# Performance work log

Hardware: AMD Instinct MI355X
Metric: run time of the kernel (lower is better)

The kernel has to match this reference:

```python
import jax, jax.numpy as jnp
import numpy as np

NUM_HEADS = 16
NUM_KV_HEADS = 4
HEAD_DIM = 128
MIN_VALUE = -1e9  # fp32 branch of the torch code


def _rotate_half_interleaved(x):
    # stack([-x[...,1::2], x[...,::2]], -1).reshape_as(x)
    x_even = x[..., ::2]
    x_odd = x[..., 1::2]
    return jnp.stack([-x_odd, x_even], axis=-1).reshape(x.shape)


def setup_inputs() -> dict:
    key = jax.random.key(0)
    ks = jax.random.split(key, 7)
    B, S, D = 2, 2048, 2048
    hidden_states = jax.random.normal(ks[0], (B, S, D), dtype=jnp.float32)
    # realistic rope tables
    inv_freq = 1.0 / (100000.0 ** (np.arange(0, HEAD_DIM, 2, dtype=np.float32) / HEAD_DIM))
    t = np.arange(S, dtype=np.float32)
    freqs = np.outer(t, inv_freq)  # (S, HEAD_DIM/2)
    emb = np.repeat(freqs, 2, axis=-1)  # interleaved layout (S, HEAD_DIM)
    cos = jnp.asarray(np.cos(emb), dtype=jnp.float32)
    sin = jnp.asarray(np.sin(emb), dtype=jnp.float32)
    scale = 0.02
    Wq = jax.random.normal(ks[1], (D, D), dtype=jnp.float32) * scale
    Wk = jax.random.normal(ks[2], (D, NUM_KV_HEADS * HEAD_DIM), dtype=jnp.float32) * scale
    Wv = jax.random.normal(ks[3], (D, NUM_KV_HEADS * HEAD_DIM), dtype=jnp.float32) * scale
    Wo = jax.random.normal(ks[4], (D, D), dtype=jnp.float32) * scale
    return {"hidden_states": hidden_states, "cos": cos, "sin": sin,
            "Wq": Wq, "Wk": Wk, "Wv": Wv, "Wo": Wo}


def reference(hidden_states, cos, sin, Wq, Wk, Wv, Wo):
    B, S, D = hidden_states.shape
    H, KV, hd = NUM_HEADS, NUM_KV_HEADS, HEAD_DIM
    q = (hidden_states @ Wq).reshape(B, S, H, hd)
    k = (hidden_states @ Wk).reshape(B, S, KV, hd)
    v = (hidden_states @ Wv).reshape(B, S, KV, hd)

    # RoPE: cos/sin (S, hd) unsqueezed to (S, 1, hd) broadcasting over heads
    c = cos[:, None, :]
    s = sin[:, None, :]
    q = q * c + _rotate_half_interleaved(q) * s
    k = k * c + _rotate_half_interleaved(k) * s

    # repeat_kv (GQA expansion): (B,S,KV,hd) -> (B,S,H,hd)
    rep = H // KV
    k = jnp.repeat(k, rep, axis=2)
    v = jnp.repeat(v, rep, axis=2)

    scores = jnp.einsum('bqhd,bkhd->bhqk', q, k) / jnp.sqrt(jnp.float32(hd))
    causal = jnp.triu(jnp.ones((S, S), dtype=bool), k=1)
    scores = jnp.where(causal[None, None], scores + MIN_VALUE, scores)
    probs = jax.nn.softmax(scores, axis=-1)
    attn = jnp.einsum('bhqk,bkhd->bqhd', probs, v).reshape(B, S, D)
    out = attn @ Wo
    return out
```

## Files before the change

### kernel.cpp

```cpp
#include <hip/hip_runtime.h>

typedef unsigned short u16;
typedef unsigned int u32;
typedef __bf16 bf16x8 __attribute__((ext_vector_type(8)));
typedef float f32x4 __attribute__((ext_vector_type(4)));

__device__ __forceinline__ u16 f2bf(float f) {
  union { float f; u32 u; } v; v.f = f;
  u32 r = v.u + 0x7fffu + ((v.u >> 16) & 1u);
  return (u16)(r >> 16);
}

__device__ __forceinline__ bf16x8 ldb128(const u16* p) {
  return *reinterpret_cast<const bf16x8*>(p);
}

__device__ __forceinline__ f32x4 mfma16(bf16x8 a, bf16x8 b, f32x4 c) {
  return __builtin_amdgcn_mfma_f32_16x16x32_bf16(a, b, c, 0, 0, 0);
}

typedef const __attribute__((address_space(1))) u32* gas_p;
typedef __attribute__((address_space(3))) u32* las_p;
__device__ __forceinline__ void gld_lds16(const void* g, void* l) {
  __builtin_amdgcn_global_load_lds((gas_p)(unsigned long long)g,
                                   (las_p)(u32)(unsigned long long)l, 16, 0, 0);
}

__global__ __launch_bounds__(256) void cvt_f32_bf16(const float4* __restrict__ in,
                                                    uint2* __restrict__ out) {
  int i = blockIdx.x * 256 + threadIdx.x;
  float4 v = in[i];
  uint2 r;
  r.x = (u32)f2bf(v.x) | ((u32)f2bf(v.y) << 16);
  r.y = (u32)f2bf(v.z) | ((u32)f2bf(v.w) << 16);
  out[i] = r;
}

__global__ __launch_bounds__(256) void transp_cvt(const float* __restrict__ in,
                                                  u16* __restrict__ out, int R, int C) {
  __shared__ float tile[32][33];
  int n0 = blockIdx.x * 32, k0 = blockIdx.y * 32;
  int tx = threadIdx.x, ty = threadIdx.y;
#pragma unroll
  for (int i = 0; i < 32; i += 8) tile[ty + i][tx] = in[(k0 + ty + i) * C + n0 + tx];
  __syncthreads();
#pragma unroll
  for (int i = 0; i < 32; i += 8) out[(n0 + ty + i) * R + k0 + tx] = f2bf(tile[tx][ty + i]);
}

template<int BN, int WM, int WN, int MODE, int LOADS>
__global__ __launch_bounds__(512) void gemm_pipe(
    const u16* __restrict__ A, const u16* __restrict__ Bt,
    int M, int N, int K,
    const float* __restrict__ cosb, const float* __restrict__ sinb,
    u16* __restrict__ Qb, u16* __restrict__ Kb, u16* __restrict__ Vt,
    float* __restrict__ outf) {
  constexpr int BM = 256;
  constexpr int WTM = BM / WM;
  constexpr int WTN = BN / WN;
  constexpr int MR = WTM / 16;
  constexpr int NR = WTN / 16;
  constexpr int PA = (BM / 8) / 8;
  constexpr int PB = (BN / 8) / 8;

  __shared__ u16 As[2][BM][64];
  __shared__ u16 Bs[2][BN][64];

  const int tid = threadIdx.x;
  const int wv = tid >> 6, lane = tid & 63;
  const int c = lane & 15, g = lane >> 4;
  const int swz = (c & 7) << 4;

  const int nwg = gridDim.x * gridDim.y;
  const int obid = blockIdx.y * gridDim.x + blockIdx.x;
  const int bid = (obid & 7) * (nwg >> 3) + (obid >> 3);
  const int m0 = (bid / gridDim.x) * BM;
  const int n0 = (bid % gridDim.x) * BN;

  const int wm = wv / WN, wn = wv % WN;

  const int lr = lane >> 3;
  const int lc8 = ((lane & 7) ^ lr) * 8;

  f32x4 acc[MR][NR] = {};
  const int NT = K >> 6;

  auto STAGE = [&](int buf, int t) {
    const int k0 = t * 64;
#pragma unroll
    for (int i = 0; i < PA; i++) {
      const int ch = wv * PA + i;
      gld_lds16(A + (long)(m0 + ch * 8 + lr) * K + k0 + lc8, &As[buf][ch * 8][0]);
    }
#pragma unroll
    for (int i = 0; i < PB; i++) {
      const int ch = wv * PB + i;
      gld_lds16(Bt + (long)(n0 + ch * 8 + lr) * K + k0 + lc8, &Bs[buf][ch * 8][0]);
    }
  };

  auto COMPUTE = [&](int buf) {
#pragma unroll
    for (int kk = 0; kk < 2; kk++) {
      bf16x8 af[MR], bfr[NR];
#pragma unroll
      for (int i = 0; i < MR; i++)
        af[i] = ldb128(&As[buf][wm * WTM + i * 16 + c][((kk * 64 + g * 16) ^ swz) >> 1]);
#pragma unroll
      for (int j = 0; j < NR; j++)
        bfr[j] = ldb128(&Bs[buf][wn * WTN + j * 16 + c][((kk * 64 + g * 16) ^ swz) >> 1]);
      __builtin_amdgcn_s_setprio(1);
#pragma unroll
      for (int i = 0; i < MR; i++)
#pragma unroll
        for (int j = 0; j < NR; j++)
          acc[i][j] = mfma16(af[i], bfr[j], acc[i][j]);
      __builtin_amdgcn_s_setprio(0);
    }
  };

  STAGE(0, 0);
  for (int t = 0; t < NT - 1; ++t) {
    STAGE((t + 1) & 1, t + 1);
    asm volatile("s_waitcnt vmcnt(%0)" :: "i"(LOADS) : "memory");
    __builtin_amdgcn_s_barrier();
    __builtin_amdgcn_sched_barrier(0);
    COMPUTE(t & 1);
    __builtin_amdgcn_sched_barrier(0);
    asm volatile("" ::: "memory");
    __builtin_amdgcn_s_barrier();
  }
  asm volatile("s_waitcnt vmcnt(0)" ::: "memory");
  __builtin_amdgcn_s_barrier();
  COMPUTE((NT - 1) & 1);

  const float inv_sqrt_hd = 0.08838834764831845f;
#pragma unroll
  for (int i = 0; i < MR; i++) {
#pragma unroll
    for (int j = 0; j < NR; j++) {
      const int ncol = n0 + wn * WTN + j * 16 + c;
#pragma unroll
      for (int r = 0; r < 4; r++) {
        const int m = m0 + wm * WTM + i * 16 + g * 4 + r;
        float val = acc[i][j][r];
        if (MODE == 1) {
          outf[(long)m * N + ncol] = val;
          continue;
        }
        const int s = m & 2047;
        if (ncol < 2048) {
          const int d = ncol & 127;
          float ct = cosb[s * 128 + d], st = sinb[s * 128 + d];
          float pr = __shfl_xor(val, 1, 64);
          float rot = (ncol & 1) ? pr : -pr;
          Qb[m * 2048 + ncol] = f2bf((val * ct + rot * st) * inv_sqrt_hd);
        } else if (ncol < 2560) {
          const int d = ncol & 127;
          float ct = cosb[s * 128 + d], st = sinb[s * 128 + d];
          float pr = __shfl_xor(val, 1, 64);
          float rot = (ncol & 1) ? pr : -pr;
          Kb[m * 512 + (ncol - 2048)] = f2bf(val * ct + rot * st);
        } else {
          const int bb = m >> 11;
          Vt[(bb * 512 + (ncol - 2560)) * 2048 + s] = f2bf(val);
        }
      }
    }
  }
}

__global__ __launch_bounds__(256) void attn_fwd(
    const u16* __restrict__ Qb, const u16* __restrict__ Kb,
    const u16* __restrict__ Vt, u16* __restrict__ attnb) {
  __shared__ u16 Ks[64 * 128];
  __shared__ u16 Vs[128 * 64];
  __shared__ u16 Pl[4][16 * 64];
  const int tid = threadIdx.x;
  const int wv = tid >> 6, lane = tid & 63;
  const int c = lane & 15, g = lane >> 4;
  const int qt = 31 - (int)blockIdx.x;
  const int h = blockIdx.y, b = blockIdx.z;
  const int kvh = h >> 2;
  const int q = qt * 64 + wv * 16 + c;
  const int swz = (c & 7) << 4;

  bf16x8 qf[4];
  const u16* qptr = Qb + ((b << 11) + q) * 2048 + h * 128 + g * 8;
#pragma unroll
  for (int dc = 0; dc < 4; dc++) qf[dc] = ldb128(qptr + dc * 32);

  f32x4 oacc[8] = {};
  float m_run = -1e30f, l_run = 0.f;

  const int krow = wv * 16 + g;
  const int vrow = wv * 32 + (lane >> 3);
  const u16* Kg = Kb + kvh * 128;
  const u16* Vg = Vt + (b * 512 + kvh * 128) * 2048;

  for (int kt = 0; kt <= qt; kt++) {
    const int k0 = kt * 64;
#pragma unroll
    for (int i = 0; i < 4; i++) {
      const int r = krow + i * 4;
      gld_lds16(Kg + ((long)(b * 2048 + k0 + r)) * 512 + ((c ^ (r & 7)) * 8),
                &Ks[(wv * 4 + i) * 512]);
    }
#pragma unroll
    for (int i = 0; i < 4; i++) {
      const int r = vrow + i * 8;
      gld_lds16(Vg + (long)r * 2048 + k0 + (((lane & 7) ^ (r & 7)) * 8),
                &Vs[(wv * 4 + i) * 512]);
    }
    __syncthreads();

    f32x4 t[4] = {};
#pragma unroll
    for (int kf = 0; kf < 4; kf++) {
#pragma unroll
      for (int dc = 0; dc < 4; dc++) {
        const bf16x8 kfr = ldb128(&Ks[(kf * 16 + c) * 128 + (((dc * 64 + g * 16) ^ swz) >> 1)]);
        t[kf] = mfma16(kfr, qf[dc], t[kf]);
      }
    }
    if (kt == qt) {
#pragma unroll
      for (int kf = 0; kf < 4; kf++)
#pragma unroll
        for (int r = 0; r < 4; r++)
          if (k0 + kf * 16 + g * 4 + r > q) t[kf][r] = -1e30f;
    }
    float pmax = -1e30f;
#pragma unroll
    for (int kf = 0; kf < 4; kf++)
#pragma unroll
      for (int r = 0; r < 4; r++) pmax = fmaxf(pmax, t[kf][r]);
    pmax = fmaxf(pmax, __shfl_xor(pmax, 16, 64));
    pmax = fmaxf(pmax, __shfl_xor(pmax, 32, 64));
    const float mnew = fmaxf(m_run, pmax);
    const float scale = __expf(m_run - mnew);
    float psum = 0.f;
#pragma unroll
    for (int kf = 0; kf < 4; kf++) {
      float p0 = __expf(t[kf][0] - mnew), p1 = __expf(t[kf][1] - mnew);
      float p2 = __expf(t[kf][2] - mnew), p3 = __expf(t[kf][3] - mnew);
      psum += (p0 + p1) + (p2 + p3);
      u32* pw = (u32*)&Pl[wv][c * 64 + (((kf * 32 + g * 8) ^ swz) >> 1)];
      pw[0] = (u32)f2bf(p0) | ((u32)f2bf(p1) << 16);
      pw[1] = (u32)f2bf(p2) | ((u32)f2bf(p3) << 16);
    }
    psum += __shfl_xor(psum, 16, 64);
    psum += __shfl_xor(psum, 32, 64);
    l_run = l_run * scale + psum;
    m_run = mnew;
#pragma unroll
    for (int df = 0; df < 8; df++) oacc[df] *= scale;

    const bf16x8 pb0 = ldb128(&Pl[wv][c * 64 + (((g * 16) ^ swz) >> 1)]);
    const bf16x8 pb1 = ldb128(&Pl[wv][c * 64 + (((64 + g * 16) ^ swz) >> 1)]);
#pragma unroll
    for (int df = 0; df < 8; df++) {
      const int vb = (df * 16 + c) * 64;
      oacc[df] = mfma16(ldb128(&Vs[vb + (((g * 16) ^ swz) >> 1)]), pb0, oacc[df]);
      oacc[df] = mfma16(ldb128(&Vs[vb + (((64 + g * 16) ^ swz) >> 1)]), pb1, oacc[df]);
    }
    __syncthreads();
  }

  const float rinv = 1.f / l_run;
  const int obase = ((b << 11) + q) * 2048 + h * 128;
#pragma unroll
  for (int df = 0; df < 8; df++)
#pragma unroll
    for (int r = 0; r < 4; r++)
      attnb[obase + df * 16 + g * 4 + r] = f2bf(oacc[df][r] * rinv);
}

extern "C" void kernel_launch(void* const* d_in, const int* in_sizes, int n_in,
                              void* d_out, int out_size, void* d_ws, size_t ws_size,
                              hipStream_t stream) {
  const float* X    = (const float*)d_in[0];
  const float* cosb = (const float*)d_in[1];
  const float* sinb = (const float*)d_in[2];
  const float* Wq   = (const float*)d_in[3];
  const float* Wk   = (const float*)d_in[4];
  const float* Wv   = (const float*)d_in[5];
  const float* Wo   = (const float*)d_in[6];

  char* ws = (char*)d_ws;
  u16* Xb    = (u16*)(ws);
  u16* Wt    = (u16*)(ws + 16777216);
  u16* Wot   = (u16*)(ws + 29360128);
  u16* Qb    = (u16*)(ws + 37748736);
  u16* Kb    = (u16*)(ws + 54525952);
  u16* Vt    = (u16*)(ws + 58720256);
  u16* attnb = Xb;

  cvt_f32_bf16<<<dim3(8192), dim3(256), 0, stream>>>((const float4*)X, (uint2*)Xb);
  transp_cvt<<<dim3(64, 64), dim3(32, 8), 0, stream>>>(Wq, Wt, 2048, 2048);
  transp_cvt<<<dim3(16, 64), dim3(32, 8), 0, stream>>>(Wk, Wt + 2048 * 2048, 2048, 512);
  transp_cvt<<<dim3(16, 64), dim3(32, 8), 0, stream>>>(Wv, Wt + 2560 * 2048, 2048, 512);
  transp_cvt<<<dim3(64, 64), dim3(32, 8), 0, stream>>>(Wo, Wot, 2048, 2048);
  gemm_pipe<256, 2, 4, 0, 8><<<dim3(12, 16), dim3(512), 0, stream>>>(
      Xb, Wt, 4096, 3072, 2048, cosb, sinb, Qb, Kb, Vt, nullptr);
  attn_fwd<<<dim3(32, 16, 2), dim3(256), 0, stream>>>(Qb, Kb, Vt, attnb);
  gemm_pipe<128, 4, 2, 1, 6><<<dim3(16, 16), dim3(512), 0, stream>>>(
      attnb, Wot, 4096, 2048, 2048, nullptr, nullptr, nullptr, nullptr, nullptr,
      (float*)d_out);
}
```

Baseline: 395.1 us.

## Double-buffer attention KV tiles, process two query sub-tiles per wave, vectorize epilogues

The attention kernel now handles 128 queries per block, with two 16-row query sub-tiles per wave. This reuses each K/V LDS fragment across twice the MFMAs, and the K/V tiles are double-buffered so global-to-LDS loads overlap compute. Softmax switches to exp2 with log2(e) folded into the Q scale. Output, V-transpose and P stores use packed bf16 conversions and wider writes. The QKV GEMM tile changes to 192 columns with a different grid. The costs are higher register and LDS use (launch bounds set to 2 blocks per CU) and a halved attention grid, which may leave CUs underused.

After: 331.7 us. -16.1%, faster.

```diff
diff --git a/kernel.cpp b/kernel.cpp
--- a/kernel.cpp
+++ b/kernel.cpp
@@ -9,6 +9,12 @@
   union { float f; u32 u; } v; v.f = f;
   u32 r = v.u + 0x7fffu + ((v.u >> 16) & 1u);
   return (u16)(r >> 16);
+}
+
+__device__ __forceinline__ u32 pack2(float a, float b) {
+  union { __bf16 h[2]; u32 u; } x;
+  x.h[0] = (__bf16)a; x.h[1] = (__bf16)b;
+  return x.u;
 }
 
 __device__ __forceinline__ bf16x8 ldb128(const u16* p) {
@@ -134,146 +140,198 @@
   __builtin_amdgcn_s_barrier();
   COMPUTE((NT - 1) & 1);
 
-  const float inv_sqrt_hd = 0.08838834764831845f;
+  const float q_scale = 0.12751743f;
 #pragma unroll
   for (int i = 0; i < MR; i++) {
 #pragma unroll
     for (int j = 0; j < NR; j++) {
       const int ncol = n0 + wn * WTN + j * 16 + c;
-#pragma unroll
-      for (int r = 0; r < 4; r++) {
-        const int m = m0 + wm * WTM + i * 16 + g * 4 + r;
-        float val = acc[i][j][r];
-        if (MODE == 1) {
-          outf[(long)m * N + ncol] = val;
-          continue;
+      if (MODE == 1) {
+#pragma unroll
+        for (int r = 0; r < 4; r++) {
+          const int m = m0 + wm * WTM + i * 16 + g * 4 + r;
+          outf[(long)m * N + ncol] = acc[i][j][r];
         }
-        const int s = m & 2047;
-        if (ncol < 2048) {
+        continue;
+      }
+      if (ncol < 2560) {
+#pragma unroll
+        for (int r = 0; r < 4; r++) {
+          const int m = m0 + wm * WTM + i * 16 + g * 4 + r;
+          const int s = m & 2047;
           const int d = ncol & 127;
+          float val = acc[i][j][r];
           float ct = cosb[s * 128 + d], st = sinb[s * 128 + d];
           float pr = __shfl_xor(val, 1, 64);
           float rot = (ncol & 1) ? pr : -pr;
-          Qb[m * 2048 + ncol] = f2bf((val * ct + rot * st) * inv_sqrt_hd);
-        } else if (ncol < 2560) {
-          const int d = ncol & 127;
-          float ct = cosb[s * 128 + d], st = sinb[s * 128 + d];
-          float pr = __shfl_xor(val, 1, 64);
-          float rot = (ncol & 1) ? pr : -pr;
-          Kb[m * 512 + (ncol - 2048)] = f2bf(val * ct + rot * st);
-        } else {
-          const int bb = m >> 11;
-          Vt[(bb * 512 + (ncol - 2560)) * 2048 + s] = f2bf(val);
+          float rp = val * ct + rot * st;
+          if (ncol < 2048) Qb[m * 2048 + ncol] = f2bf(rp * q_scale);
+          else             Kb[m * 512 + (ncol - 2048)] = f2bf(rp);
         }
+      } else {
+        const int m_base = m0 + wm * WTM + i * 16 + g * 4;
+        const int bb = m_base >> 11;
+        const int srow = m_base & 2047;
+        uint2 pv;
+        pv.x = pack2(acc[i][j][0], acc[i][j][1]);
+        pv.y = pack2(acc[i][j][2], acc[i][j][3]);
+        *(uint2*)&Vt[(bb * 512 + (ncol - 2560)) * 2048 + srow] = pv;
       }
     }
   }
 }
 
-__global__ __launch_bounds__(256) void attn_fwd(
+__global__ __launch_bounds__(256, 2) void attn_fwd(
     const u16* __restrict__ Qb, const u16* __restrict__ Kb,
     const u16* __restrict__ Vt, u16* __restrict__ attnb) {
-  __shared__ u16 Ks[64 * 128];
-  __shared__ u16 Vs[128 * 64];
-  __shared__ u16 Pl[4][16 * 64];
+  __shared__ u16 Ks[2][64 * 128];
+  __shared__ u16 Vs[2][128 * 64];
+  __shared__ u16 Pl[4][2][16 * 64];
   const int tid = threadIdx.x;
   const int wv = tid >> 6, lane = tid & 63;
   const int c = lane & 15, g = lane >> 4;
-  const int qt = 31 - (int)blockIdx.x;
+  const int qt = 15 - (int)blockIdx.x;
   const int h = blockIdx.y, b = blockIdx.z;
   const int kvh = h >> 2;
-  const int q = qt * 64 + wv * 16 + c;
+  const int qbase = qt * 128 + wv * 32;
   const int swz = (c & 7) << 4;
 
-  bf16x8 qf[4];
-  const u16* qptr = Qb + ((b << 11) + q) * 2048 + h * 128 + g * 8;
-#pragma unroll
-  for (int dc = 0; dc < 4; dc++) qf[dc] = ldb128(qptr + dc * 32);
-
-  f32x4 oacc[8] = {};
-  float m_run = -1e30f, l_run = 0.f;
+  bf16x8 qf0[4], qf1[4];
+  {
+    const u16* qp0 = Qb + ((b << 11) + qbase + c) * 2048 + h * 128 + g * 8;
+#pragma unroll
+    for (int dc = 0; dc < 4; dc++) qf0[dc] = ldb128(qp0 + dc * 32);
+    const u16* qp1 = qp0 + 16 * 2048;
+#pragma unroll
+    for (int dc = 0; dc < 4; dc++) qf1[dc] = ldb128(qp1 + dc * 32);
+  }
+
+  f32x4 oacc0[8] = {}, oacc1[8] = {};
+  float m0r = -1e30f, l0r = 0.f, m1r = -1e30f, l1r = 0.f;
 
   const int krow = wv * 16 + g;
   const int vrow = wv * 32 + (lane >> 3);
   const u16* Kg = Kb + kvh * 128;
   const u16* Vg = Vt + (b * 512 + kvh * 128) * 2048;
-
-  for (int kt = 0; kt <= qt; kt++) {
-    const int k0 = kt * 64;
+  const int NKV = 2 * qt + 2;
+
+  auto STAGE = [&](int buf, int t) {
+    const int k0 = t * 64;
 #pragma unroll
     for (int i = 0; i < 4; i++) {
       const int r = krow + i * 4;
       gld_lds16(Kg + ((long)(b * 2048 + k0 + r)) * 512 + ((c ^ (r & 7)) * 8),
-                &Ks[(wv * 4 + i) * 512]);
+                &Ks[buf][(wv * 4 + i) * 512]);
     }
 #pragma unroll
     for (int i = 0; i < 4; i++) {
       const int r = vrow + i * 8;
       gld_lds16(Vg + (long)r * 2048 + k0 + (((lane & 7) ^ (r & 7)) * 8),
-                &Vs[(wv * 4 + i) * 512]);
-    }
-    __syncthreads();
-
-    f32x4 t[4] = {};
+                &Vs[buf][(wv * 4 + i) * 512]);
+    }
+  };
+
+  STAGE(0, 0);
+  for (int kt = 0; kt < NKV; kt++) {
+    const int buf = kt & 1;
+    const int k0 = kt * 64;
+    if (kt + 1 < NKV) {
+      STAGE(buf ^ 1, kt + 1);
+      asm volatile("s_waitcnt vmcnt(8)" ::: "memory");
+    } else {
+      asm volatile("s_waitcnt vmcnt(0)" ::: "memory");
+    }
+    __builtin_amdgcn_s_barrier();
+    __builtin_amdgcn_sched_barrier(0);
+
+    f32x4 t0[4] = {}, t1[4] = {};
 #pragma unroll
     for (int kf = 0; kf < 4; kf++) {
 #pragma unroll
       for (int dc = 0; dc < 4; dc++) {
-        const bf16x8 kfr = ldb128(&Ks[(kf * 16 + c) * 128 + (((dc * 64 + g * 16) ^ swz) >> 1)]);
-        t[kf] = mfma16(kfr, qf[dc], t[kf]);
+        const bf16x8 kfr =
+            ldb128(&Ks[buf][(kf * 16 + c) * 128 + (((dc * 64 + g * 16) ^ swz) >> 1)]);
+        t0[kf] = mfma16(kfr, qf0[dc], t0[kf]);
+        t1[kf] = mfma16(kfr, qf1[dc], t1[kf]);
       }
     }
-    if (kt == qt) {
+    if (kt >= NKV - 2) {
+      const int q0 = qbase + c, q1 = q0 + 16;
 #pragma unroll
       for (int kf = 0; kf < 4; kf++)
 #pragma unroll
-        for (int r = 0; r < 4; r++)
-          if (k0 + kf * 16 + g * 4 + r > q) t[kf][r] = -1e30f;
-    }
-    float pmax = -1e30f;
-#pragma unroll
-    for (int kf = 0; kf < 4; kf++)
-#pragma unroll
-      for (int r = 0; r < 4; r++) pmax = fmaxf(pmax, t[kf][r]);
-    pmax = fmaxf(pmax, __shfl_xor(pmax, 16, 64));
-    pmax = fmaxf(pmax, __shfl_xor(pmax, 32, 64));
-    const float mnew = fmaxf(m_run, pmax);
-    const float scale = __expf(m_run - mnew);
-    float psum = 0.f;
-#pragma unroll
-    for (int kf = 0; kf < 4; kf++) {
-      float p0 = __expf(t[kf][0] - mnew), p1 = __expf(t[kf][1] - mnew);
-      float p2 = __expf(t[kf][2] - mnew), p3 = __expf(t[kf][3] - mnew);
-      psum += (p0 + p1) + (p2 + p3);
-      u32* pw = (u32*)&Pl[wv][c * 64 + (((kf * 32 + g * 8) ^ swz) >> 1)];
-      pw[0] = (u32)f2bf(p0) | ((u32)f2bf(p1) << 16);
-      pw[1] = (u32)f2bf(p2) | ((u32)f2bf(p3) << 16);
-    }
-    psum += __shfl_xor(psum, 16, 64);
-    psum += __shfl_xor(psum, 32, 64);
-    l_run = l_run * scale + psum;
-    m_run = mnew;
-#pragma unroll
-    for (int df = 0; df < 8; df++) oacc[df] *= scale;
-
-    const bf16x8 pb0 = ldb128(&Pl[wv][c * 64 + (((g * 16) ^ swz) >> 1)]);
-    const bf16x8 pb1 = ldb128(&Pl[wv][c * 64 + (((64 + g * 16) ^ swz) >> 1)]);
+        for (int r = 0; r < 4; r++) {
+          const int key = k0 + kf * 16 + g * 4 + r;
+          if (key > q0) t0[kf][r] = -1e30f;
+          if (key > q1) t1[kf][r] = -1e30f;
+        }
+    }
+#pragma unroll
+    for (int s = 0; s < 2; s++) {
+      f32x4* t = s ? t1 : t0;
+      float& mr = s ? m1r : m0r;
+      float& lr_ = s ? l1r : l0r;
+      f32x4* oa = s ? oacc1 : oacc0;
+      float pmax = -1e30f;
+#pragma unroll
+      for (int kf = 0; kf < 4; kf++)
+#pragma unroll
+        for (int r = 0; r < 4; r++) pmax = fmaxf(pmax, t[kf][r]);
+      pmax = fmaxf(pmax, __shfl_xor(pmax, 16, 64));
+      pmax = fmaxf(pmax, __shfl_xor(pmax, 32, 64));
+      const float mnew = fmaxf(mr, pmax);
+      const float scale = __builtin_amdgcn_exp2f(mr - mnew);
+      float psum = 0.f;
+#pragma unroll
+      for (int kf = 0; kf < 4; kf++) {
+        float p0 = __builtin_amdgcn_exp2f(t[kf][0] - mnew);
+        float p1 = __builtin_amdgcn_exp2f(t[kf][1] - mnew);
+        float p2 = __builtin_amdgcn_exp2f(t[kf][2] - mnew);
+        float p3 = __builtin_amdgcn_exp2f(t[kf][3] - mnew);
+        psum += (p0 + p1) + (p2 + p3);
+        u32* pw = (u32*)&Pl[wv][s][c * 64 + (((kf * 32 + g * 8) ^ swz) >> 1)];
+        pw[0] = pack2(p0, p1);
+        pw[1] = pack2(p2, p3);
+      }
+      psum += __shfl_xor(psum, 16, 64);
+      psum += __shfl_xor(psum, 32, 64);
+      lr_ = lr_ * scale + psum;
+      mr = mnew;
+#pragma unroll
+      for (int df = 0; df < 8; df++) oa[df] *= scale;
+    }
+
+    const bf16x8 pa0 = ldb128(&Pl[wv][0][c * 64 + (((g * 16) ^ swz) >> 1)]);
+    const bf16x8 pa1 = ldb128(&Pl[wv][0][c * 64 + (((64 + g * 16) ^ swz) >> 1)]);
+    const bf16x8 pb0 = ldb128(&Pl[wv][1][c * 64 + (((g * 16) ^ swz) >> 1)]);
+    const bf16x8 pb1 = ldb128(&Pl[wv][1][c * 64 + (((64 + g * 16) ^ swz) >> 1)]);
 #pragma unroll
     for (int df = 0; df < 8; df++) {
       const int vb = (df * 16 + c) * 64;
-      oacc[df] = mfma16(ldb128(&Vs[vb + (((g * 16) ^ swz) >> 1)]), pb0, oacc[df]);
-      oacc[df] = mfma16(ldb128(&Vs[vb + (((64 + g * 16) ^ swz) >> 1)]), pb1, oacc[df]);
-    }
-    __syncthreads();
-  }
-
-  const float rinv = 1.f / l_run;
-  const int obase = ((b << 11) + q) * 2048 + h * 128;
-#pragma unroll
-  for (int df = 0; df < 8; df++)
-#pragma unroll
-    for (int r = 0; r < 4; r++)
-      attnb[obase + df * 16 + g * 4 + r] = f2bf(oacc[df][r] * rinv);
+      const bf16x8 v0 = ldb128(&Vs[buf][vb + (((g * 16) ^ swz) >> 1)]);
+      const bf16x8 v1 = ldb128(&Vs[buf][vb + (((64 + g * 16) ^ swz) >> 1)]);
+      oacc0[df] = mfma16(v0, pa0, oacc0[df]);
+      oacc0[df] = mfma16(v1, pa1, oacc0[df]);
+      oacc1[df] = mfma16(v0, pb0, oacc1[df]);
+      oacc1[df] = mfma16(v1, pb1, oacc1[df]);
+    }
+    __builtin_amdgcn_sched_barrier(0);
+    asm volatile("" ::: "memory");
+    __builtin_amdgcn_s_barrier();
+  }
+
+  const float ri0 = 1.f / l0r, ri1 = 1.f / l1r;
+  const long ob0 = ((long)(b << 11) + qbase + c) * 2048 + h * 128 + g * 4;
+#pragma unroll
+  for (int df = 0; df < 8; df++) {
+    uint2 o0, o1;
+    o0.x = pack2(oacc0[df][0] * ri0, oacc0[df][1] * ri0);
+    o0.y = pack2(oacc0[df][2] * ri0, oacc0[df][3] * ri0);
+    o1.x = pack2(oacc1[df][0] * ri1, oacc1[df][1] * ri1);
+    o1.y = pack2(oacc1[df][2] * ri1, oacc1[df][3] * ri1);
+    *(uint2*)&attnb[ob0 + df * 16] = o0;
+    *(uint2*)&attnb[ob0 + 16 * 2048 + df * 16] = o1;
+  }
 }
 
 extern "C" void kernel_launch(void* const* d_in, const int* in_sizes, int n_in,
@@ -301,9 +359,9 @@
   transp_cvt<<<dim3(16, 64), dim3(32, 8), 0, stream>>>(Wk, Wt + 2048 * 2048, 2048, 512);
   transp_cvt<<<dim3(16, 64), dim3(32, 8), 0, stream>>>(Wv, Wt + 2560 * 2048, 2048, 512);
   transp_cvt<<<dim3(64, 64), dim3(32, 8), 0, stream>>>(Wo, Wot, 2048, 2048);
-  gemm_pipe<256, 2, 4, 0, 8><<<dim3(12, 16), dim3(512), 0, stream>>>(
+  gemm_pipe<192, 2, 4, 0, 7><<<dim3(16, 16), dim3(512), 0, stream>>>(
       Xb, Wt, 4096, 3072, 2048, cosb, sinb, Qb, Kb, Vt, nullptr);
-  attn_fwd<<<dim3(32, 16, 2), dim3(256), 0, stream>>>(Qb, Kb, Vt, attnb);
+  attn_fwd<<<dim3(16, 16, 2), dim3(256), 0, stream>>>(Qb, Kb, Vt, attnb);
   gemm_pipe<128, 4, 2, 1, 6><<<dim3(16, 16), dim3(512), 0, stream>>>(
       attnb, Wot, 4096, 2048, 2048, nullptr, nullptr, nullptr, nullptr, nullptr,
       (float*)d_out);
```
